# Optimization experiments

Measured on AMD Instinct MI355X. Metric: run time of the kernel, lower is better.

Reference implementation:

```python
import jax, jax.numpy as jnp
import numpy as np
from jax.ops import segment_sum

N_NODES = 50000
N_EDGES = 800000
D_IN = 256
D_HID2 = 256   # hidden_channels * 2
D_HID = 128    # hidden_channels
D_MLP = 64     # hidden_channels // 2
D_OUT = 64


def setup_inputs() -> dict:
    key = jax.random.key(0)
    ks = jax.random.split(key, 16)
    def glorot(k, shape):
        lim = float(np.sqrt(6.0 / (shape[0] + shape[1])))
        return jax.random.uniform(k, shape, jnp.float32, -lim, lim)
    x = jax.random.normal(ks[0], (N_NODES, D_IN), jnp.float32)
    edge_index = jax.random.randint(ks[1], (2, N_EDGES), 0, N_NODES, jnp.int64)
    return {
        "x": x,
        "edge_index": edge_index,
        "W1": glorot(ks[2], (D_IN, D_HID2)),   "b1": jnp.zeros((D_HID2,), jnp.float32),
        "W2": glorot(ks[3], (D_HID2, D_HID2)), "b2": jnp.zeros((D_HID2,), jnp.float32),
        "W3": glorot(ks[4], (D_HID2, D_HID)),  "b3": jnp.zeros((D_HID,), jnp.float32),
        "mW1": glorot(ks[5], (D_HID, D_MLP)),  "mb1": jnp.zeros((D_MLP,), jnp.float32),
        "mW2": glorot(ks[6], (D_MLP, D_OUT)),  "mb2": jnp.zeros((D_OUT,), jnp.float32),
    }


def _graph_conv(x, src, dst, W, b, n_nodes):
    # DGL GraphConv with norm='both': h = D_in^{-1/2} * A @ (D_out^{-1/2} * x @ W) + b
    ones = jnp.ones((src.shape[0],), x.dtype)
    deg_out = jnp.clip(segment_sum(ones, src, num_segments=n_nodes), 1.0)
    deg_in = jnp.clip(segment_sum(ones, dst, num_segments=n_nodes), 1.0)
    h = (x * jax.lax.rsqrt(deg_out)[:, None]) @ W          # [N, d_out]
    agg = segment_sum(h[src], dst, num_segments=n_nodes)    # gather-scatter over edges
    return agg * jax.lax.rsqrt(deg_in)[:, None] + b


def reference(x, edge_index, W1, b1, W2, b2, W3, b3, mW1, mb1, mW2, mb2):
    src, dst = edge_index[0], edge_index[1]
    n = x.shape[0]
    # eval mode: dropout is identity
    h = jax.nn.relu(_graph_conv(x, src, dst, W1, b1, n))
    h = jax.nn.relu(_graph_conv(h, src, dst, W2, b2, n))
    h_last = jax.nn.relu(_graph_conv(h, src, dst, W3, b3, n))
    out = jax.nn.relu(h_last @ mW1 + mb1) @ mW2 + mb2
    return (out, h_last)
```

## Files before the change

kernel.cpp:

```cpp
#include <hip/hip_runtime.h>
#include <hip/hip_bf16.h>

typedef __hip_bfloat16 bf16;
typedef __attribute__((ext_vector_type(8))) __bf16 bfrag;
typedef __attribute__((ext_vector_type(4))) float f32x4;

#define N_NODES 50000
#define N_EDGES 800000

__device__ __forceinline__ unsigned short f2bf(float f) {
    bf16 h = __float2bfloat16(f);
    return *reinterpret_cast<unsigned short*>(&h);
}

__device__ __forceinline__ uint4 zero4() { uint4 z; z.x = z.y = z.z = z.w = 0u; return z; }

__global__ void detect_kernel(const unsigned short* __restrict__ xb,
                              const int* __restrict__ ei,
                              int* __restrict__ flags) {
    __shared__ int s_insane, s_nonzero;
    int t = threadIdx.x;
    if (t == 0) { s_insane = 0; s_nonzero = 0; }
    __syncthreads();
    unsigned short h = xb[2 * t];
    int e = (h >> 7) & 0xFF;
    if (!(e == 0 || (e >= 90 && e <= 150))) atomicOr(&s_insane, 1);
    if (ei[2 * t + 1] != 0) atomicOr(&s_nonzero, 1);
    __syncthreads();
    if (t == 0) { flags[0] = s_insane ? 1 : 0; flags[1] = s_nonzero ? 0 : 1; }
}

__device__ __forceinline__ void load_edge(const int* __restrict__ ei, int fl64,
                                          int e, int& s, int& d) {
    if (fl64) { s = ei[2 * e]; d = ei[2 * N_EDGES + 2 * e]; }
    else      { s = ei[e];     d = ei[N_EDGES + e]; }
}

__device__ __forceinline__ float rdf(const void* p, int off, int f32) {
    return f32 ? ((const float*)p)[off] : (float)((const bf16*)p)[off];
}

__global__ void cvt_all_kernel(const void* W1, const void* W2, const void* W3,
                               const void* mW1, const void* mW2,
                               const void* b1, const void* b2, const void* b3,
                               const void* mb1, const void* mb2,
                               const int* __restrict__ flags,
                               unsigned short* __restrict__ WT,
                               float* __restrict__ biasd) {
    int i = blockIdx.x * 256 + threadIdx.x;
    if (i >= 176896) return;
    const int f32 = flags[0];
    if (i < 163840) {
        const void* s; int local, N;
        if      (i <  65536) { s = W1; local = i;          N = 256; }
        else if (i < 131072) { s = W2; local = i -  65536; N = 256; }
        else                 { s = W3; local = i - 131072; N = 128; }
        int n = local >> 8, k = local & 255;
        WT[i] = f2bf(rdf(s, k * N + n, f32));
    } else if (i < 172032) {
        int local = i - 163840;
        int n = local >> 7, k = local & 127;
        WT[i] = f2bf(rdf(mW1, k * 64 + n, f32));
    } else if (i < 176128) {
        int local = i - 172032;
        int n = local >> 6, k = local & 63;
        WT[i] = f2bf(rdf(mW2, k * 64 + n, f32));
    } else {
        int local = i - 176128;
        const void* s; int off;
        if      (local < 256) { s = b1;  off = local; }
        else if (local < 512) { s = b2;  off = local - 256; }
        else if (local < 640) { s = b3;  off = local - 512; }
        else if (local < 704) { s = mb1; off = local - 640; }
        else                  { s = mb2; off = local - 704; }
        biasd[local] = rdf(s, off, f32);
    }
}

__global__ void cvt_x_kernel(const void* __restrict__ x,
                             const int* __restrict__ flags,
                             unsigned short* __restrict__ xbf) {
    int i = blockIdx.x * 256 + threadIdx.x;
    if (i >= (N_NODES * 256) / 4) return;
    if (flags[0]) {
        float4 v = ((const float4*)x)[i];
        ushort4 o;
        o.x = f2bf(v.x); o.y = f2bf(v.y); o.z = f2bf(v.z); o.w = f2bf(v.w);
        ((ushort4*)xbf)[i] = o;
    } else {
        ((ushort4*)xbf)[i] = ((const ushort4*)x)[i];
    }
}

__global__ void place_kernel(const int* __restrict__ ei,
                             const int* __restrict__ flags,
                             int* __restrict__ cntS, int* __restrict__ cntD,
                             int* __restrict__ esrc_pad) {
    int e = blockIdx.x * blockDim.x + threadIdx.x;
    if (e >= N_EDGES) return;
    int s, d; load_edge(ei, flags[1], e, s, d);
    atomicAdd(&cntS[s], 1);
    int pos = atomicAdd(&cntD[d], 1);
    if (pos < 64) esrc_pad[(d << 6) + pos] = s;
}

__global__ void rsq_kernel(const int* __restrict__ cntS,
                           const int* __restrict__ cntD,
                           float* __restrict__ sOut, float* __restrict__ sIn,
                           int n) {
    int i = blockIdx.x * blockDim.x + threadIdx.x;
    if (i < n) {
        sOut[i] = rsqrtf((float)max(cntS[i], 1));
        sIn[i]  = rsqrtf((float)max(cntD[i], 1));
    }
}

__launch_bounds__(256)
__global__ void mfma_gemm_kernel(const unsigned short* __restrict__ X,
                                 const unsigned short* __restrict__ WT,
                                 const float* __restrict__ rowscale,
                                 unsigned short* __restrict__ C,
                                 int M, int N) {
    constexpr int K = 256;
    __shared__ unsigned short Xs[128][40];
    __shared__ unsigned short Ws[128][40];
    const int tid  = threadIdx.x;
    const int lane = tid & 63;
    const int w    = tid >> 6;
    const int wr   = (w >> 1) * 64;
    const int wc   = (w & 1) * 64;
    const int lrow = lane & 15;
    const int koff = (lane >> 4) * 8;
    const int row0 = blockIdx.y * 128;
    const int col0 = blockIdx.x * 128;

    const int r0 = tid >> 2, q0 = tid & 3;
    const int r1 = r0 + 64;
    const int gr0 = row0 + r0, gr1 = row0 + r1;

    uint4 xv0 = (gr0 < M) ? *(const uint4*)(X + (size_t)gr0 * K + q0 * 8) : zero4();
    uint4 xv1 = (gr1 < M) ? *(const uint4*)(X + (size_t)gr1 * K + q0 * 8) : zero4();
    uint4 wv0 = *(const uint4*)(WT + (size_t)(col0 + r0) * K + q0 * 8);
    uint4 wv1 = *(const uint4*)(WT + (size_t)(col0 + r1) * K + q0 * 8);

    f32x4 acc[4][4] = {};

    for (int k0 = 0; k0 < K; k0 += 32) {
        *(uint4*)&Xs[r0][q0 * 8] = xv0;
        *(uint4*)&Xs[r1][q0 * 8] = xv1;
        *(uint4*)&Ws[r0][q0 * 8] = wv0;
        *(uint4*)&Ws[r1][q0 * 8] = wv1;
        __syncthreads();

        const int k1 = k0 + 32;
        if (k1 < K) {
            xv0 = (gr0 < M) ? *(const uint4*)(X + (size_t)gr0 * K + k1 + q0 * 8) : zero4();
            xv1 = (gr1 < M) ? *(const uint4*)(X + (size_t)gr1 * K + k1 + q0 * 8) : zero4();
            wv0 = *(const uint4*)(WT + (size_t)(col0 + r0) * K + k1 + q0 * 8);
            wv1 = *(const uint4*)(WT + (size_t)(col0 + r1) * K + k1 + q0 * 8);
        }

        bfrag af[4], bv[4];
#pragma unroll
        for (int i = 0; i < 4; i++)
            af[i] = *(const bfrag*)&Xs[wr + i * 16 + lrow][koff];
#pragma unroll
        for (int j = 0; j < 4; j++)
            bv[j] = *(const bfrag*)&Ws[wc + j * 16 + lrow][koff];
#pragma unroll
        for (int i = 0; i < 4; i++)
#pragma unroll
            for (int j = 0; j < 4; j++)
                acc[i][j] = __builtin_amdgcn_mfma_f32_16x16x32_bf16(
                    af[i], bv[j], acc[i][j], 0, 0, 0);
        __syncthreads();
    }

#pragma unroll
    for (int i = 0; i < 4; i++) {
#pragma unroll
        for (int r = 0; r < 4; r++) {
            int row = row0 + wr + i * 16 + ((lane >> 4) * 4) + r;
            if (row >= M) continue;
            float s = rowscale[row];
#pragma unroll
            for (int j = 0; j < 4; j++) {
                int col = col0 + wc + j * 16 + lrow;
                C[(size_t)row * N + col] = f2bf(acc[i][j][r] * s);
            }
        }
    }
}

__launch_bounds__(256)
__global__ void mfma_mlp2_kernel(const unsigned short* __restrict__ X,
                                 const unsigned short* __restrict__ WT1,
                                 const unsigned short* __restrict__ WT2,
                                 const float* __restrict__ b1,
                                 const float* __restrict__ b2,
                                 float* __restrict__ out, int M) {
    __shared__ unsigned short Xs[128][136];
    __shared__ unsigned short W1s[64][136];
    __shared__ unsigned short W2s[64][72];
    const int tid  = threadIdx.x;
    const int lane = tid & 63;
    const int w    = tid >> 6;
    const int lrow = lane & 15;
    const int koff = (lane >> 4) * 8;
    const int row0 = blockIdx.x * 128;

#pragma unroll
    for (int i = 0; i < 8; i++) {
        int c = tid + i * 256;
        int r = c >> 4, q = c & 15;
        int gr = row0 + r;
        uint4 v = (gr < M) ? *(const uint4*)(X + (size_t)gr * 128 + q * 8) : zero4();
        *(uint4*)&Xs[r][q * 8] = v;
    }
#pragma unroll
    for (int i = 0; i < 4; i++) {
        int c = tid + i * 256;
        int n = c >> 4, q = c & 15;
        *(uint4*)&W1s[n][q * 8] = *(const uint4*)(WT1 + (size_t)n * 128 + q * 8);
    }
#pragma unroll
    for (int i = 0; i < 2; i++) {
        int c = tid + i * 256;
        int n = c >> 3, q = c & 7;
        *(uint4*)&W2s[n][q * 8] = *(const uint4*)(WT2 + (size_t)n * 64 + q * 8);
    }
    __syncthreads();

    f32x4 acc[2][4] = {};
#pragma unroll
    for (int k0 = 0; k0 < 128; k0 += 32) {
        bfrag af[2], bv[4];
#pragma unroll
        for (int i = 0; i < 2; i++)
            af[i] = *(const bfrag*)&Xs[w * 32 + i * 16 + lrow][k0 + koff];
#pragma unroll
        for (int j = 0; j < 4; j++)
            bv[j] = *(const bfrag*)&W1s[j * 16 + lrow][k0 + koff];
#pragma unroll
        for (int i = 0; i < 2; i++)
#pragma unroll
            for (int j = 0; j < 4; j++)
                acc[i][j] = __builtin_amdgcn_mfma_f32_16x16x32_bf16(
                    af[i], bv[j], acc[i][j], 0, 0, 0);
    }
    __syncthreads();

#pragma unroll
    for (int i = 0; i < 2; i++) {
#pragma unroll
        for (int r = 0; r < 4; r++) {
            int row = w * 32 + i * 16 + ((lane >> 4) * 4) + r;
#pragma unroll
            for (int j = 0; j < 4; j++) {
                int col = j * 16 + lrow;
                Xs[row][col] = f2bf(fmaxf(acc[i][j][r] + b1[col], 0.0f));
            }
        }
    }
    __syncthreads();

    f32x4 acc2[2][4] = {};
#pragma unroll
    for (int k0 = 0; k0 < 64; k0 += 32) {
        bfrag af[2], bv[4];
#pragma unroll
        for (int i = 0; i < 2; i++)
            af[i] = *(const bfrag*)&Xs[w * 32 + i * 16 + lrow][k0 + koff];
#pragma unroll
        for (int j = 0; j < 4; j++)
            bv[j] = *(const bfrag*)&W2s[j * 16 + lrow][k0 + koff];
#pragma unroll
        for (int i = 0; i < 2; i++)
#pragma unroll
            for (int j = 0; j < 4; j++)
                acc2[i][j] = __builtin_amdgcn_mfma_f32_16x16x32_bf16(
                    af[i], bv[j], acc2[i][j], 0, 0, 0);
    }

#pragma unroll
    for (int i = 0; i < 2; i++) {
#pragma unroll
        for (int r = 0; r < 4; r++) {
            int row = row0 + w * 32 + i * 16 + ((lane >> 4) * 4) + r;
            if (row >= M) continue;
#pragma unroll
            for (int j = 0; j < 4; j++) {
                int col = j * 16 + lrow;
                out[(size_t)row * 64 + col] = acc2[i][j][r] + b2[col];
            }
        }
    }
}

__device__ __forceinline__ void acc_pair(unsigned int u, float& a0, float& a1) {
    a0 += __uint_as_float(u << 16);
    a1 += __uint_as_float(u & 0xffff0000u);
}

template <int LQ, int OUT>
__launch_bounds__(256)
__global__ void gather_bf16_kernel(const int* __restrict__ cnt,
                                   const int* __restrict__ esrc_pad,
                                   const unsigned short* __restrict__ H,
                                   const float* __restrict__ sIn,
                                   const float* __restrict__ bias,
                                   float* __restrict__ Yf,
                                   unsigned short* __restrict__ Yb, int nNodes) {
    constexpr int NPB = 256 / LQ;
    constexpr int D = LQ * 8;
    const int tid = threadIdx.x;
    const int node = blockIdx.x * NPB + tid / LQ;
    const int lane = tid % LQ;
    if (node >= nNodes) return;
    const uint4* __restrict__ H4 = (const uint4*)H;
    const int* __restrict__ ep = esrc_pad + (node << 6);

    float a0 = 0.f, a1 = 0.f, a2 = 0.f, a3 = 0.f;
    float a4 = 0.f, a5 = 0.f, a6 = 0.f, a7 = 0.f;
    const int cn = min(cnt[node], 64);
    int j = 0;
    for (; j + 2 <= cn; j += 2) {
        uint4 u = H4[(size_t)ep[j] * LQ + lane];
        uint4 v = H4[(size_t)ep[j + 1] * LQ + lane];
        acc_pair(u.x, a0, a1); acc_pair(u.y, a2, a3);
        acc_pair(u.z, a4, a5); acc_pair(u.w, a6, a7);
        acc_pair(v.x, a0, a1); acc_pair(v.y, a2, a3);
        acc_pair(v.z, a4, a5); acc_pair(v.w, a6, a7);
    }
    if (j < cn) {
        uint4 u = H4[(size_t)ep[j] * LQ + lane];
        acc_pair(u.x, a0, a1); acc_pair(u.y, a2, a3);
        acc_pair(u.z, a4, a5); acc_pair(u.w, a6, a7);
    }
    const float sc = sIn[node];
    const float* bp = bias + lane * 8;
    float4 b0 = *(const float4*)(bp);
    float4 b1 = *(const float4*)(bp + 4);
    float r0 = fmaxf(fmaf(a0, sc, b0.x), 0.0f);
    float r1 = fmaxf(fmaf(a1, sc, b0.y), 0.0f);
    float r2 = fmaxf(fmaf(a2, sc, b0.z), 0.0f);
    float r3 = fmaxf(fmaf(a3, sc, b0.w), 0.0f);
    float r4 = fmaxf(fmaf(a4, sc, b1.x), 0.0f);
    float r5 = fmaxf(fmaf(a5, sc, b1.y), 0.0f);
    float r6 = fmaxf(fmaf(a6, sc, b1.z), 0.0f);
    float r7 = fmaxf(fmaf(a7, sc, b1.w), 0.0f);
    if (OUT == 2) {
        float* yp = Yf + (size_t)node * D + lane * 8;
        float4 o0 = {r0, r1, r2, r3};
        float4 o1 = {r4, r5, r6, r7};
        *(float4*)(yp)     = o0;
        *(float4*)(yp + 4) = o1;
    }
    {
        unsigned short* yp = Yb + (size_t)node * D + lane * 8;
        ushort4 o0, o1;
        o0.x = f2bf(r0); o0.y = f2bf(r1); o0.z = f2bf(r2); o0.w = f2bf(r3);
        o1.x = f2bf(r4); o1.y = f2bf(r5); o1.z = f2bf(r6); o1.w = f2bf(r7);
        *(ushort4*)(yp)     = o0;
        *(ushort4*)(yp + 4) = o1;
    }
}

extern "C" void kernel_launch(void* const* d_in, const int* in_sizes, int n_in,
                              void* d_out, int out_size, void* d_ws, size_t ws_size,
                              hipStream_t stream) {
    const void* x  = d_in[0];
    const int*  ei = (const int*)d_in[1];
    const void *W1 = d_in[2],  *b1 = d_in[3];
    const void *W2 = d_in[4],  *b2 = d_in[5];
    const void *W3 = d_in[6],  *b3 = d_in[7];
    const void *mW1 = d_in[8], *mb1 = d_in[9];
    const void *mW2 = d_in[10],*mb2 = d_in[11];

    float* out   = (float*)d_out;
    float* out_h = out + (size_t)N_NODES * 64;

    float* ws = (float*)d_ws;
    size_t off = 0;
    int*   flags  = (int*)(ws + off); off += 64;
    int*   cntS   = (int*)(ws + off); off += N_NODES;
    int*   cntD   = (int*)(ws + off); off += N_NODES;
    int*   esrc_p = (int*)(ws + off); off += (size_t)N_NODES * 64;
    float* sOut   = ws + off;         off += N_NODES;
    float* sIn    = ws + off;         off += N_NODES;
    float* biasd  = ws + off;         off += 768;
    off = (off + 63) & ~(size_t)63;
    unsigned short* WT  = (unsigned short*)(ws + off); off += 88448;
    unsigned short* Gbf = (unsigned short*)(ws + off); off += (size_t)N_NODES * 128;
    unsigned short* Hbf = (unsigned short*)(ws + off); off += (size_t)N_NODES * 128;
    unsigned short* hob = (unsigned short*)(ws + off); off += (size_t)N_NODES * 64;

    const int M = N_NODES;
    const dim3 blk(256);
    const int gE  = (N_EDGES + 255) / 256;
    const int gy128 = (M + 127) / 128;

    detect_kernel<<<1, blk, 0, stream>>>((const unsigned short*)x, ei, flags);
    cvt_all_kernel<<<(176896 + 255) / 256, blk, 0, stream>>>(
        W1, W2, W3, mW1, mW2, b1, b2, b3, mb1, mb2, flags, WT, biasd);
    cvt_x_kernel<<<(N_NODES * 256 / 4 + 255) / 256, blk, 0, stream>>>(x, flags, Gbf);

    hipMemsetAsync(cntS, 0, 2 * N_NODES * sizeof(int), stream);
    place_kernel<<<gE, blk, 0, stream>>>(ei, flags, cntS, cntD, esrc_p);
    rsq_kernel<<<(M + 255) / 256, blk, 0, stream>>>(cntS, cntD, sOut, sIn, M);

    mfma_gemm_kernel<<<dim3(2, gy128), blk, 0, stream>>>(Gbf, WT, sOut, Hbf, M, 256);
    gather_bf16_kernel<32, 0><<<(M + 7) / 8, blk, 0, stream>>>(
        cntD, esrc_p, Hbf, sIn, biasd, nullptr, Gbf, M);

    mfma_gemm_kernel<<<dim3(2, gy128), blk, 0, stream>>>(Gbf, WT + 65536, sOut, Hbf, M, 256);
    gather_bf16_kernel<32, 0><<<(M + 7) / 8, blk, 0, stream>>>(
        cntD, esrc_p, Hbf, sIn, biasd + 256, nullptr, Gbf, M);

    mfma_gemm_kernel<<<dim3(1, gy128), blk, 0, stream>>>(Gbf, WT + 131072, sOut, Hbf, M, 128);
    gather_bf16_kernel<16, 2><<<(M + 15) / 16, blk, 0, stream>>>(
        cntD, esrc_p, Hbf, sIn, biasd + 512, out_h, hob, M);

    mfma_mlp2_kernel<<<gy128, blk, 0, stream>>>(
        hob, WT + 163840, WT + 172032, biasd + 640, biasd + 704, out, M);
}
```

Measured before the change: 414.1 us.

## Split neighbor gather into column slabs and store edge sources as u16

The aggregation kernel now gives each block a fixed column slab of the feature rows, spread over many destination nodes, using a 2D grid. The goal is a smaller hot working set of H per block to improve cache reuse. Padded source indices are stored as 16-bit values, which halves the index traffic and workspace. This depends on the node count staying under 65536. Each node's index list is now read once per slab, and each lane group fetches shorter contiguous segments per row.

```diff
diff --git a/kernel.cpp b/kernel.cpp
--- a/kernel.cpp
+++ b/kernel.cpp
@@ -95,13 +95,13 @@
 __global__ void place_kernel(const int* __restrict__ ei,
                              const int* __restrict__ flags,
                              int* __restrict__ cntS, int* __restrict__ cntD,
-                             int* __restrict__ esrc_pad) {
+                             unsigned short* __restrict__ esrc_pad) {
     int e = blockIdx.x * blockDim.x + threadIdx.x;
     if (e >= N_EDGES) return;
     int s, d; load_edge(ei, flags[1], e, s, d);
     atomicAdd(&cntS[s], 1);
     int pos = atomicAdd(&cntD[d], 1);
-    if (pos < 64) esrc_pad[(d << 6) + pos] = s;
+    if (pos < 64) esrc_pad[(d << 6) + pos] = (unsigned short)s;
 }
 
 __global__ void rsq_kernel(const int* __restrict__ cntS,
@@ -302,43 +302,44 @@
     a1 += __uint_as_float(u & 0xffff0000u);
 }
 
-template <int LQ, int OUT>
+template <int LPS, int OUT>
 __launch_bounds__(256)
-__global__ void gather_bf16_kernel(const int* __restrict__ cnt,
-                                   const int* __restrict__ esrc_pad,
+__global__ void gather_slab_kernel(const int* __restrict__ cnt,
+                                   const unsigned short* __restrict__ esrc_pad,
                                    const unsigned short* __restrict__ H,
                                    const float* __restrict__ sIn,
                                    const float* __restrict__ bias,
                                    float* __restrict__ Yf,
                                    unsigned short* __restrict__ Yb, int nNodes) {
-    constexpr int NPB = 256 / LQ;
+    constexpr int NPB = 256 / LPS;
+    constexpr int LQ = LPS * 8;
     constexpr int D = LQ * 8;
-    const int tid = threadIdx.x;
-    const int node = blockIdx.x * NPB + tid / LQ;
-    const int lane = tid % LQ;
+    const int tid  = threadIdx.x;
+    const int node = blockIdx.y * NPB + tid / LPS;
+    const int col  = blockIdx.x * LPS + (tid % LPS);
     if (node >= nNodes) return;
     const uint4* __restrict__ H4 = (const uint4*)H;
-    const int* __restrict__ ep = esrc_pad + (node << 6);
+    const unsigned short* __restrict__ ep = esrc_pad + (node << 6);
 
     float a0 = 0.f, a1 = 0.f, a2 = 0.f, a3 = 0.f;
     float a4 = 0.f, a5 = 0.f, a6 = 0.f, a7 = 0.f;
     const int cn = min(cnt[node], 64);
     int j = 0;
     for (; j + 2 <= cn; j += 2) {
-        uint4 u = H4[(size_t)ep[j] * LQ + lane];
-        uint4 v = H4[(size_t)ep[j + 1] * LQ + lane];
+        uint4 u = H4[(size_t)ep[j] * LQ + col];
+        uint4 v = H4[(size_t)ep[j + 1] * LQ + col];
         acc_pair(u.x, a0, a1); acc_pair(u.y, a2, a3);
         acc_pair(u.z, a4, a5); acc_pair(u.w, a6, a7);
         acc_pair(v.x, a0, a1); acc_pair(v.y, a2, a3);
         acc_pair(v.z, a4, a5); acc_pair(v.w, a6, a7);
     }
     if (j < cn) {
-        uint4 u = H4[(size_t)ep[j] * LQ + lane];
+        uint4 u = H4[(size_t)ep[j] * LQ + col];
         acc_pair(u.x, a0, a1); acc_pair(u.y, a2, a3);
         acc_pair(u.z, a4, a5); acc_pair(u.w, a6, a7);
     }
     const float sc = sIn[node];
-    const float* bp = bias + lane * 8;
+    const float* bp = bias + col * 8;
     float4 b0 = *(const float4*)(bp);
     float4 b1 = *(const float4*)(bp + 4);
     float r0 = fmaxf(fmaf(a0, sc, b0.x), 0.0f);
@@ -350,14 +351,14 @@
     float r6 = fmaxf(fmaf(a6, sc, b1.z), 0.0f);
     float r7 = fmaxf(fmaf(a7, sc, b1.w), 0.0f);
     if (OUT == 2) {
-        float* yp = Yf + (size_t)node * D + lane * 8;
+        float* yp = Yf + (size_t)node * D + col * 8;
         float4 o0 = {r0, r1, r2, r3};
         float4 o1 = {r4, r5, r6, r7};
         *(float4*)(yp)     = o0;
         *(float4*)(yp + 4) = o1;
     }
     {
-        unsigned short* yp = Yb + (size_t)node * D + lane * 8;
+        unsigned short* yp = Yb + (size_t)node * D + col * 8;
         ushort4 o0, o1;
         o0.x = f2bf(r0); o0.y = f2bf(r1); o0.z = f2bf(r2); o0.w = f2bf(r3);
         o1.x = f2bf(r4); o1.y = f2bf(r5); o1.z = f2bf(r6); o1.w = f2bf(r7);
@@ -385,7 +386,8 @@
     int*   flags  = (int*)(ws + off); off += 64;
     int*   cntS   = (int*)(ws + off); off += N_NODES;
     int*   cntD   = (int*)(ws + off); off += N_NODES;
-    int*   esrc_p = (int*)(ws + off); off += (size_t)N_NODES * 64;
+    unsigned short* esrc_p = (unsigned short*)(ws + off);
+    off += (size_t)N_NODES * 32;
     float* sOut   = ws + off;         off += N_NODES;
     float* sIn    = ws + off;         off += N_NODES;
     float* biasd  = ws + off;         off += 768;
@@ -410,15 +412,15 @@
     rsq_kernel<<<(M + 255) / 256, blk, 0, stream>>>(cntS, cntD, sOut, sIn, M);
 
     mfma_gemm_kernel<<<dim3(2, gy128), blk, 0, stream>>>(Gbf, WT, sOut, Hbf, M, 256);
-    gather_bf16_kernel<32, 0><<<(M + 7) / 8, blk, 0, stream>>>(
+    gather_slab_kernel<4, 0><<<dim3(8, (M + 63) / 64), blk, 0, stream>>>(
         cntD, esrc_p, Hbf, sIn, biasd, nullptr, Gbf, M);
 
     mfma_gemm_kernel<<<dim3(2, gy128), blk, 0, stream>>>(Gbf, WT + 65536, sOut, Hbf, M, 256);
-    gather_bf16_kernel<32, 0><<<(M + 7) / 8, blk, 0, stream>>>(
+    gather_slab_kernel<4, 0><<<dim3(8, (M + 63) / 64), blk, 0, stream>>>(
         cntD, esrc_p, Hbf, sIn, biasd + 256, nullptr, Gbf, M);
 
     mfma_gemm_kernel<<<dim3(1, gy128), blk, 0, stream>>>(Gbf, WT + 131072, sOut, Hbf, M, 128);
-    gather_bf16_kernel<16, 2><<<(M + 15) / 16, blk, 0, stream>>>(
+    gather_slab_kernel<2, 2><<<dim3(8, (M + 127) / 128), blk, 0, stream>>>(
         cntD, esrc_p, Hbf, sIn, biasd + 512, out_h, hob, M);
 
     mfma_mlp2_kernel<<<gy128, blk, 0, stream>>>(
```

After: 611.8 us. 1.48x slower.

## Fuse x conversion into first GEMM, shrink edge lists to u16, unroll gather

Applied to the files above, without the earlier changes.

Removes the separate fp32-to-bf16 conversion pass over x and has the first GEMM read fp32 rows directly, converting them while loading the tile. The padded per-node source lists are stored as 16-bit indices, since node ids fit below 65536, which halves index traffic in the gather kernels. The gather inner loop is unrolled to four edges per iteration to keep more loads in flight. The first GEMM now reads twice the bytes of x, once per column block, and the 16-bit indices depend on the node count staying under 65536.

```diff
diff --git a/kernel.cpp b/kernel.cpp
--- a/kernel.cpp
+++ b/kernel.cpp
@@ -77,31 +77,16 @@
     }
 }
 
-__global__ void cvt_x_kernel(const void* __restrict__ x,
-                             const int* __restrict__ flags,
-                             unsigned short* __restrict__ xbf) {
-    int i = blockIdx.x * 256 + threadIdx.x;
-    if (i >= (N_NODES * 256) / 4) return;
-    if (flags[0]) {
-        float4 v = ((const float4*)x)[i];
-        ushort4 o;
-        o.x = f2bf(v.x); o.y = f2bf(v.y); o.z = f2bf(v.z); o.w = f2bf(v.w);
-        ((ushort4*)xbf)[i] = o;
-    } else {
-        ((ushort4*)xbf)[i] = ((const ushort4*)x)[i];
-    }
-}
-
 __global__ void place_kernel(const int* __restrict__ ei,
                              const int* __restrict__ flags,
                              int* __restrict__ cntS, int* __restrict__ cntD,
-                             int* __restrict__ esrc_pad) {
+                             unsigned short* __restrict__ esrc_pad) {
     int e = blockIdx.x * blockDim.x + threadIdx.x;
     if (e >= N_EDGES) return;
     int s, d; load_edge(ei, flags[1], e, s, d);
     atomicAdd(&cntS[s], 1);
     int pos = atomicAdd(&cntD[d], 1);
-    if (pos < 64) esrc_pad[(d << 6) + pos] = s;
+    if (pos < 64) esrc_pad[(d << 6) + pos] = (unsigned short)s;
 }
 
 __global__ void rsq_kernel(const int* __restrict__ cntS,
@@ -115,8 +100,24 @@
     }
 }
 
+__device__ __forceinline__ uint4 ld8_bf16(const unsigned short* p) {
+    return *(const uint4*)p;
+}
+__device__ __forceinline__ uint4 ld8_f32(const float* p) {
+    float4 a = *(const float4*)(p);
+    float4 b = *(const float4*)(p + 4);
+    uint4 r;
+    r.x = ((unsigned)f2bf(a.y) << 16) | f2bf(a.x);
+    r.y = ((unsigned)f2bf(a.w) << 16) | f2bf(a.z);
+    r.z = ((unsigned)f2bf(b.y) << 16) | f2bf(b.x);
+    r.w = ((unsigned)f2bf(b.w) << 16) | f2bf(b.z);
+    return r;
+}
+
+template <bool DUALX>
 __launch_bounds__(256)
-__global__ void mfma_gemm_kernel(const unsigned short* __restrict__ X,
+__global__ void mfma_gemm_kernel(const void* __restrict__ Xv,
+                                 const int* __restrict__ flags,
                                  const unsigned short* __restrict__ WT,
                                  const float* __restrict__ rowscale,
                                  unsigned short* __restrict__ C,
@@ -133,15 +134,24 @@
     const int koff = (lane >> 4) * 8;
     const int row0 = blockIdx.y * 128;
     const int col0 = blockIdx.x * 128;
+    const bool xf32 = DUALX && (flags[0] != 0);
+    const unsigned short* Xb = (const unsigned short*)Xv;
+    const float* Xf = (const float*)Xv;
 
     const int r0 = tid >> 2, q0 = tid & 3;
     const int r1 = r0 + 64;
     const int gr0 = row0 + r0, gr1 = row0 + r1;
 
-    uint4 xv0 = (gr0 < M) ? *(const uint4*)(X + (size_t)gr0 * K + q0 * 8) : zero4();
-    uint4 xv1 = (gr1 < M) ? *(const uint4*)(X + (size_t)gr1 * K + q0 * 8) : zero4();
-    uint4 wv0 = *(const uint4*)(WT + (size_t)(col0 + r0) * K + q0 * 8);
-    uint4 wv1 = *(const uint4*)(WT + (size_t)(col0 + r1) * K + q0 * 8);
+    uint4 xv0, xv1, wv0, wv1;
+    {
+        int e = q0 * 8;
+        xv0 = (gr0 < M) ? (xf32 ? ld8_f32(Xf + (size_t)gr0 * K + e)
+                                : ld8_bf16(Xb + (size_t)gr0 * K + e)) : zero4();
+        xv1 = (gr1 < M) ? (xf32 ? ld8_f32(Xf + (size_t)gr1 * K + e)
+                                : ld8_bf16(Xb + (size_t)gr1 * K + e)) : zero4();
+        wv0 = *(const uint4*)(WT + (size_t)(col0 + r0) * K + e);
+        wv1 = *(const uint4*)(WT + (size_t)(col0 + r1) * K + e);
+    }
 
     f32x4 acc[4][4] = {};
 
@@ -154,10 +164,13 @@
 
         const int k1 = k0 + 32;
         if (k1 < K) {
-            xv0 = (gr0 < M) ? *(const uint4*)(X + (size_t)gr0 * K + k1 + q0 * 8) : zero4();
-            xv1 = (gr1 < M) ? *(const uint4*)(X + (size_t)gr1 * K + k1 + q0 * 8) : zero4();
-            wv0 = *(const uint4*)(WT + (size_t)(col0 + r0) * K + k1 + q0 * 8);
-            wv1 = *(const uint4*)(WT + (size_t)(col0 + r1) * K + k1 + q0 * 8);
+            int e = k1 + q0 * 8;
+            xv0 = (gr0 < M) ? (xf32 ? ld8_f32(Xf + (size_t)gr0 * K + e)
+                                    : ld8_bf16(Xb + (size_t)gr0 * K + e)) : zero4();
+            xv1 = (gr1 < M) ? (xf32 ? ld8_f32(Xf + (size_t)gr1 * K + e)
+                                    : ld8_bf16(Xb + (size_t)gr1 * K + e)) : zero4();
+            wv0 = *(const uint4*)(WT + (size_t)(col0 + r0) * K + e);
+            wv1 = *(const uint4*)(WT + (size_t)(col0 + r1) * K + e);
         }
 
         bfrag af[4], bv[4];
@@ -301,11 +314,17 @@
     a0 += __uint_as_float(u << 16);
     a1 += __uint_as_float(u & 0xffff0000u);
 }
+__device__ __forceinline__ void acc4(uint4 u, float& a0, float& a1, float& a2,
+                                     float& a3, float& a4, float& a5,
+                                     float& a6, float& a7) {
+    acc_pair(u.x, a0, a1); acc_pair(u.y, a2, a3);
+    acc_pair(u.z, a4, a5); acc_pair(u.w, a6, a7);
+}
 
 template <int LQ, int OUT>
 __launch_bounds__(256)
 __global__ void gather_bf16_kernel(const int* __restrict__ cnt,
-                                   const int* __restrict__ esrc_pad,
+                                   const unsigned short* __restrict__ esrc_pad,
                                    const unsigned short* __restrict__ H,
                                    const float* __restrict__ sIn,
                                    const float* __restrict__ bias,
@@ -318,24 +337,25 @@
     const int lane = tid % LQ;
     if (node >= nNodes) return;
     const uint4* __restrict__ H4 = (const uint4*)H;
-    const int* __restrict__ ep = esrc_pad + (node << 6);
+    const unsigned short* __restrict__ ep = esrc_pad + (node << 6);
 
     float a0 = 0.f, a1 = 0.f, a2 = 0.f, a3 = 0.f;
     float a4 = 0.f, a5 = 0.f, a6 = 0.f, a7 = 0.f;
     const int cn = min(cnt[node], 64);
     int j = 0;
-    for (; j + 2 <= cn; j += 2) {
+    for (; j + 4 <= cn; j += 4) {
+        uint4 u0 = H4[(size_t)ep[j]     * LQ + lane];
+        uint4 u1 = H4[(size_t)ep[j + 1] * LQ + lane];
+        uint4 u2 = H4[(size_t)ep[j + 2] * LQ + lane];
+        uint4 u3 = H4[(size_t)ep[j + 3] * LQ + lane];
+        acc4(u0, a0, a1, a2, a3, a4, a5, a6, a7);
+        acc4(u1, a0, a1, a2, a3, a4, a5, a6, a7);
+        acc4(u2, a0, a1, a2, a3, a4, a5, a6, a7);
+        acc4(u3, a0, a1, a2, a3, a4, a5, a6, a7);
+    }
+    for (; j < cn; j++) {
         uint4 u = H4[(size_t)ep[j] * LQ + lane];
-        uint4 v = H4[(size_t)ep[j + 1] * LQ + lane];
-        acc_pair(u.x, a0, a1); acc_pair(u.y, a2, a3);
-        acc_pair(u.z, a4, a5); acc_pair(u.w, a6, a7);
-        acc_pair(v.x, a0, a1); acc_pair(v.y, a2, a3);
-        acc_pair(v.z, a4, a5); acc_pair(v.w, a6, a7);
-    }
-    if (j < cn) {
-        uint4 u = H4[(size_t)ep[j] * LQ + lane];
-        acc_pair(u.x, a0, a1); acc_pair(u.y, a2, a3);
-        acc_pair(u.z, a4, a5); acc_pair(u.w, a6, a7);
+        acc4(u, a0, a1, a2, a3, a4, a5, a6, a7);
     }
     const float sc = sIn[node];
     const float* bp = bias + lane * 8;
@@ -385,7 +405,8 @@
     int*   flags  = (int*)(ws + off); off += 64;
     int*   cntS   = (int*)(ws + off); off += N_NODES;
     int*   cntD   = (int*)(ws + off); off += N_NODES;
-    int*   esrc_p = (int*)(ws + off); off += (size_t)N_NODES * 64;
+    unsigned short* esrc_p = (unsigned short*)(ws + off);
+    off += (size_t)N_NODES * 32;
     float* sOut   = ws + off;         off += N_NODES;
     float* sIn    = ws + off;         off += N_NODES;
     float* biasd  = ws + off;         off += 768;
@@ -403,21 +424,23 @@
     detect_kernel<<<1, blk, 0, stream>>>((const unsigned short*)x, ei, flags);
     cvt_all_kernel<<<(176896 + 255) / 256, blk, 0, stream>>>(
         W1, W2, W3, mW1, mW2, b1, b2, b3, mb1, mb2, flags, WT, biasd);
-    cvt_x_kernel<<<(N_NODES * 256 / 4 + 255) / 256, blk, 0, stream>>>(x, flags, Gbf);
 
     hipMemsetAsync(cntS, 0, 2 * N_NODES * sizeof(int), stream);
     place_kernel<<<gE, blk, 0, stream>>>(ei, flags, cntS, cntD, esrc_p);
     rsq_kernel<<<(M + 255) / 256, blk, 0, stream>>>(cntS, cntD, sOut, sIn, M);
 
-    mfma_gemm_kernel<<<dim3(2, gy128), blk, 0, stream>>>(Gbf, WT, sOut, Hbf, M, 256);
+    mfma_gemm_kernel<true><<<dim3(2, gy128), blk, 0, stream>>>(
+        x, flags, WT, sOut, Hbf, M, 256);
     gather_bf16_kernel<32, 0><<<(M + 7) / 8, blk, 0, stream>>>(
         cntD, esrc_p, Hbf, sIn, biasd, nullptr, Gbf, M);
 
-    mfma_gemm_kernel<<<dim3(2, gy128), blk, 0, stream>>>(Gbf, WT + 65536, sOut, Hbf, M, 256);
+    mfma_gemm_kernel<false><<<dim3(2, gy128), blk, 0, stream>>>(
+        Gbf, flags, WT + 65536, sOut, Hbf, M, 256);
     gather_bf16_kernel<32, 0><<<(M + 7) / 8, blk, 0, stream>>>(
         cntD, esrc_p, Hbf, sIn, biasd + 256, nullptr, Gbf, M);
 
-    mfma_gemm_kernel<<<dim3(1, gy128), blk, 0, stream>>>(Gbf, WT + 131072, sOut, Hbf, M, 128);
+    mfma_gemm_kernel<false><<<dim3(1, gy128), blk, 0, stream>>>(
+        Gbf, flags, WT + 131072, sOut, Hbf, M, 128);
     gather_bf16_kernel<16, 2><<<(M + 15) / 16, blk, 0, stream>>>(
         cntD, esrc_p, Hbf, sIn, biasd + 512, out_h, hob, M);
 
```

Result: no change. 417.2 us (+0.7%).
